# Kernel tuning notes

Hardware: AMD Instinct MI355X
Metric: run time of the kernel (lower is better)

Reference implementation:

```python
import jax, jax.numpy as jnp
import numpy as np
from jax import lax

B, S, D, H = 2, 2048, 1024, 16
DH = D // H
KERNELS = (3, 5)
NK = len(KERNELS)
COUT = D // NK  # channels per conv branch


def setup_inputs() -> dict:
    key = jax.random.key(0)
    ks = jax.random.split(key, 12)
    w = lambda k, shp: (jax.random.normal(k, shp, dtype=jnp.float32) * 0.02)
    inp = {
        "q": jax.random.normal(ks[0], (B, S, D), dtype=jnp.float32),
        "k": jax.random.normal(ks[1], (B, S, D), dtype=jnp.float32),
        "v": jax.random.normal(ks[2], (B, S, D), dtype=jnp.float32),
        "mask": jnp.ones((B, S, S), dtype=jnp.int32),
        "Wq": w(ks[3], (D, D)),
        "Wk": w(ks[4], (D, D)),
        "Wv": w(ks[5], (D, D)),
        "Wo": w(ks[6], (D, D)),
        "bo": jnp.zeros((D,), dtype=jnp.float32),
        "conv_w0": w(ks[7], (COUT, D, KERNELS[0])),  # OIH
        "conv_b0": jnp.zeros((COUT,), dtype=jnp.float32),
        "conv_w1": w(ks[8], (COUT, D, KERNELS[1])),
        "conv_b1": jnp.zeros((COUT,), dtype=jnp.float32),
        "gate": jnp.ones((H,), dtype=jnp.float32),
    }
    return inp


def _split_heads(x):  # [B,S,D] -> [B,H,S,DH]
    return x.reshape(B, S, H, DH).transpose(0, 2, 1, 3)


def _conv1d_same(x_ncl, w_oik, b, ksz):
    pad = ksz // 2
    y = lax.conv_general_dilated(
        x_ncl, w_oik, window_strides=(1,), padding=[(pad, pad)],
        dimension_numbers=("NCH", "OIH", "NCH"))
    return y + b[None, :, None]


def reference(q, k, v, mask, Wq, Wk, Wv, Wo, bo,
              conv_w0, conv_b0, conv_w1, conv_b1, gate):
    qh = _split_heads(q @ Wq.T)
    kh = _split_heads(k @ Wk.T)
    vh = _split_heads(v @ Wv.T)

    # conv-derived K: operate on raw k in NCL layout, concat channel-wise
    k_ncl = k.transpose(0, 2, 1)  # [B,D,S]
    c0 = _conv1d_same(k_ncl, conv_w0, conv_b0, KERNELS[0])
    c1 = _conv1d_same(k_ncl, conv_w1, conv_b1, KERNELS[1])
    k_conv = jnp.concatenate([c0, c1], axis=1).transpose(0, 2, 1)  # [B,S,D]
    kch = _split_heads(k_conv)

    g = jax.nn.sigmoid(gate).reshape(1, H, 1, 1)
    scale = 1.0 / np.sqrt(DH).astype(np.float32)
    attn = ((1.0 - g) * jnp.einsum("bhqd,bhkd->bhqk", qh, kh)
            + g * jnp.einsum("bhqd,bhkd->bhqk", qh, kch)) * scale
    attn = jnp.where(mask[:, None, :, :] == 0, jnp.float32(-1e9), attn)
    attn = jax.nn.softmax(attn, axis=-1)

    out = jnp.einsum("bhqk,bhkd->bhqd", attn, vh)  # [B,H,S,DH]
    out = out.transpose(0, 2, 1, 3).reshape(B, S, D)
    return out @ Wo.T + bo
```

## Files before the change

kernel.cpp:

```cpp
#include <hip/hip_runtime.h>
#include <math.h>

#define Bb 2
#define Ss 2048
#define Dd 1024
#define Hh 16
#define SP 2052

typedef unsigned short u16;
typedef __bf16 bf16x8 __attribute__((ext_vector_type(8)));
typedef float f32x4 __attribute__((ext_vector_type(4)));
typedef unsigned short u16x8 __attribute__((ext_vector_type(8)));

__device__ __forceinline__ u16 f2bf(float f) {
    union { float f; unsigned int u; } c; c.f = f;
    unsigned int u = c.u + 0x7FFFu + ((c.u >> 16) & 1u);
    return (u16)(u >> 16);
}

__device__ __forceinline__ u16 f2bfn(float f) {
    __bf16 h = (__bf16)f;
    union { __bf16 h; u16 u; } c; c.h = h;
    return c.u;
}

__device__ __forceinline__ float bf2f(u16 h) {
    union { unsigned int u; float f; } c; c.u = ((unsigned int)h) << 16;
    return c.f;
}

__device__ __forceinline__ void gload16(const void* g, void* l) {
    __builtin_amdgcn_global_load_lds(
        (const __attribute__((address_space(1))) void*)g,
        (__attribute__((address_space(3))) void*)l, 16, 0, 0);
}

#define PREP_WB 28676
#define PREP_IB 6156
#define PREP_MB 1024

__global__ __launch_bounds__(256) void prep_all(
    const float* __restrict__ Wq, const float* __restrict__ Wk,
    const float* __restrict__ Wv, const float* __restrict__ Wo,
    const float* __restrict__ w0, const float* __restrict__ b0,
    const float* __restrict__ w1, const float* __restrict__ b1,
    const float* __restrict__ gate,
    const float* __restrict__ q, const float* __restrict__ k, const float* __restrict__ v,
    const int* __restrict__ mask,
    u16* __restrict__ wqs, u16* __restrict__ wvb, u16* __restrict__ wob,
    u16* __restrict__ Wc0, u16* __restrict__ Wc1, float* __restrict__ bc,
    u16* __restrict__ qbf, u16* __restrict__ kbf, u16* __restrict__ vbf,
    unsigned int* __restrict__ bits, int* __restrict__ rowflags)
{
    int bid = blockIdx.x, tid = threadIdx.x;
    if (bid < PREP_WB) {
        int idx = bid * 256 + tid;
        const int NW = 1024 * 1024;
        if (idx < NW) { wqs[idx] = f2bf(Wq[idx] * 0.18033688011112042f); return; }
        idx -= NW;
        if (idx < NW) { wvb[idx] = f2bf(Wv[idx]); return; }
        idx -= NW;
        if (idx < NW) { wob[idx] = f2bf(Wo[idx]); return; }
        idx -= NW;
        if (idx < 512 * 3072) {
            int c = idx / 3072, rem = idx % 3072, t = rem >> 10, d = rem & 1023;
            float g = 1.f / (1.f + expf(-gate[c >> 6]));
            float vv = g * w0[(c * 1024 + d) * 3 + t];
            if (t == 1) vv += (1.f - g) * Wk[c * 1024 + d];
            Wc0[idx] = f2bf(vv);
            return;
        }
        idx -= 512 * 3072;
        if (idx < 512 * 5120) {
            int c = idx / 5120, rem = idx % 5120, t = rem >> 10, d = rem & 1023;
            int cg = c + 512;
            float g = 1.f / (1.f + expf(-gate[cg >> 6]));
            float vv = g * w1[(c * 1024 + d) * 5 + t];
            if (t == 2) vv += (1.f - g) * Wk[cg * 1024 + d];
            Wc1[idx] = f2bf(vv);
            return;
        }
        idx -= 512 * 5120;
        if (idx < 1024) {
            float g = 1.f / (1.f + expf(-gate[idx >> 6]));
            bc[idx] = g * (idx < 512 ? b0[idx] : b1[idx - 512]);
        }
        return;
    }
    if (bid < PREP_WB + PREP_IB) {
        int idx = (bid - PREP_WB) * 256 + tid;
        const int per = (Bb * SP * Dd) / 8;
        int which = idx / per;
        if (which >= 3) return;
        int e = (idx - which * per) * 8;
        const float* src = which == 0 ? q : which == 1 ? k : v;
        u16* dst = which == 0 ? qbf : which == 1 ? kbf : vbf;
        int rp = e >> 10, col = e & 1023;
        int b = rp / SP, r = rp - b * SP;
        u16x8 o;
        if (r >= 2 && r < SP - 2) {
            const float* s = &src[((size_t)b * Ss + (r - 2)) * Dd + col];
            float4 lo = *(const float4*)s, hi = *(const float4*)(s + 4);
            o[0] = f2bf(lo.x); o[1] = f2bf(lo.y); o[2] = f2bf(lo.z); o[3] = f2bf(lo.w);
            o[4] = f2bf(hi.x); o[5] = f2bf(hi.y); o[6] = f2bf(hi.z); o[7] = f2bf(hi.w);
        } else {
            #pragma unroll
            for (int j = 0; j < 8; j++) o[j] = 0;
        }
        *(u16x8*)&dst[e] = o;
        return;
    }
    {
        int row = (bid - PREP_WB - PREP_IB) * 4 + (tid >> 6);
        int lane = tid & 63;
        const int* mp = mask + (size_t)row * Ss + lane * 32;
        unsigned int w = 0;
        #pragma unroll
        for (int j = 0; j < 32; j += 4) {
            int4 m4 = *(const int4*)&mp[j];
            if (m4.x != 0) w |= 1u << j;
            if (m4.y != 0) w |= 1u << (j + 1);
            if (m4.z != 0) w |= 1u << (j + 2);
            if (m4.w != 0) w |= 1u << (j + 3);
        }
        bits[(size_t)row * 64 + lane] = w;
        int anyz = __any(w != 0xFFFFFFFFu);
        if (lane == 0) rowflags[row] = anyz;
    }
}

__device__ __forceinline__ void run_gemm_job(
    const u16* __restrict__ A, const u16* __restrict__ B, u16* __restrict__ C,
    int strB, int kS, int kL, int mB, int nB, int rO, int Cst,
    u16* As, u16* Bsh, int lane, int wave, int waveM, int waveN)
{
    f32x4 acc[4][4];
    #pragma unroll
    for (int i = 0; i < 4; i++)
        #pragma unroll
        for (int j = 0; j < 4; j++) acc[i][j] = (f32x4){0.f, 0.f, 0.f, 0.f};

    for (int k0 = kS; k0 < kS + kL; k0 += 32) {
        __syncthreads();
        #pragma unroll
        for (int cc = 0; cc < 2; cc++) {
            int rbase = (wave * 2 + cc) * 16;
            int r = rbase + (lane >> 2);
            int gm = mB + r;
            int grow = (gm >> 11) * SP + (gm & 2047) + rO + (k0 >> 10);
            int csrc = (lane & 3) ^ (r & 3) ^ ((r >> 2) & 3);
            gload16(A + (size_t)grow * 1024 + (k0 & 1023) + csrc * 8, &As[rbase * 32]);
            int gn = nB + r;
            gload16(B + (size_t)gn * strB + k0 + csrc * 8, &Bsh[rbase * 32]);
        }
        __syncthreads();

        bf16x8 af[4], bfr[4];
        #pragma unroll
        for (int t = 0; t < 4; t++) {
            int mrow = waveM + t * 16 + (lane & 15);
            int xm = (mrow & 3) ^ ((mrow >> 2) & 3);
            af[t] = *(const bf16x8*)&As[mrow * 32 + (((lane >> 4) ^ xm)) * 8];
            int nrow = waveN + t * 16 + (lane & 15);
            int xn = (nrow & 3) ^ ((nrow >> 2) & 3);
            bfr[t] = *(const bf16x8*)&Bsh[nrow * 32 + (((lane >> 4) ^ xn)) * 8];
        }
        #pragma unroll
        for (int mt = 0; mt < 4; mt++)
            #pragma unroll
            for (int nt = 0; nt < 4; nt++)
                acc[mt][nt] = __builtin_amdgcn_mfma_f32_16x16x32_bf16(
                    af[mt], bfr[nt], acc[mt][nt], 0, 0, 0);
    }

    #pragma unroll
    for (int mt = 0; mt < 4; mt++)
        #pragma unroll
        for (int nt = 0; nt < 4; nt++)
            #pragma unroll
            for (int r = 0; r < 4; r++) {
                int row = mB + waveM + mt * 16 + (lane >> 4) * 4 + r;
                int gcol = nB + waveN + nt * 16 + (lane & 15);
                C[(size_t)row * Cst + gcol] = f2bf(acc[mt][nt][r]);
            }
}

__global__ __launch_bounds__(256) void gemm_multi(
    const u16* __restrict__ qbf, const u16* __restrict__ kbf, const u16* __restrict__ vbf,
    const u16* __restrict__ wqs, const u16* __restrict__ wvb,
    const u16* __restrict__ Wc0, const u16* __restrict__ Wc1,
    u16* __restrict__ Qp, u16* __restrict__ Vp,
    u16* __restrict__ P0a, u16* __restrict__ P0b,
    u16* __restrict__ P1a, u16* __restrict__ P1b, u16* __restrict__ P1c)
{
    __shared__ u16 As[128 * 32];
    __shared__ u16 Bsh[128 * 32];
    int tid = threadIdx.x, lane = tid & 63, wave = tid >> 6;
    int waveM = (wave >> 1) * 64, waveN = (wave & 1) * 64;

    int bid = (blockIdx.x & 7) * 96 + (blockIdx.x >> 3);

    const u16 *A0, *B0; u16 *C0; int sB0, kS0, kL0, mB0, nB0, rO0, Cs0;
    const u16 *A1 = nullptr, *B1 = nullptr; u16 *C1 = nullptr;
    int sB1 = 0, kS1 = 0, kL1 = 0, mB1 = 0, nB1 = 0, rO1 = 0, Cs1 = 0;
    int njobs = 1;

    if (bid < 128) {
        int t = bid;
        A0 = kbf; B0 = Wc0; C0 = P0a; sB0 = 3072; kS0 = 0; kL0 = 2048;
        mB0 = (t >> 2) * 128; nB0 = (t & 3) * 128; rO0 = 1; Cs0 = 512;
    } else if (bid < 256) {
        int t = bid - 128;
        A0 = kbf; B0 = Wc1; C0 = P1a; sB0 = 5120; kS0 = 0; kL0 = 2048;
        mB0 = (t >> 2) * 128; nB0 = (t & 3) * 128; rO0 = 0; Cs0 = 512;
    } else if (bid < 384) {
        int t = bid - 256;
        A0 = kbf; B0 = Wc1; C0 = P1b; sB0 = 5120; kS0 = 2048; kL0 = 2048;
        mB0 = (t >> 2) * 128; nB0 = (t & 3) * 128; rO0 = 0; Cs0 = 512;
    } else if (bid < 512) {
        int t = bid - 384;
        A0 = kbf; B0 = Wc0; C0 = P0b; sB0 = 3072; kS0 = 2048; kL0 = 1024;
        mB0 = (t >> 2) * 128; nB0 = (t & 3) * 128; rO0 = 1; Cs0 = 512;
        A1 = kbf; B1 = Wc1; C1 = P1c; sB1 = 5120; kS1 = 4096; kL1 = 1024;
        mB1 = mB0; nB1 = nB0; rO1 = 0; Cs1 = 512;
        njobs = 2;
    } else {
        int i0 = (bid - 512) * 2, i1 = i0 + 1;
        if (i0 < 256) { A0 = qbf; B0 = wqs; C0 = Qp; }
        else { i0 -= 256; A0 = vbf; B0 = wvb; C0 = Vp; }
        sB0 = 1024; kS0 = 0; kL0 = 1024;
        mB0 = (i0 >> 3) * 128; nB0 = (i0 & 7) * 128; rO0 = 2; Cs0 = 1024;
        if (i1 < 256) { A1 = qbf; B1 = wqs; C1 = Qp; }
        else { i1 -= 256; A1 = vbf; B1 = wvb; C1 = Vp; }
        sB1 = 1024; kS1 = 0; kL1 = 1024;
        mB1 = (i1 >> 3) * 128; nB1 = (i1 & 7) * 128; rO1 = 2; Cs1 = 1024;
        njobs = 2;
    }

    run_gemm_job(A0, B0, C0, sB0, kS0, kL0, mB0, nB0, rO0, Cs0,
                 As, Bsh, lane, wave, waveM, waveN);
    if (njobs == 2)
        run_gemm_job(A1, B1, C1, sB1, kS1, kL1, mB1, nB1, rO1, Cs1,
                     As, Bsh, lane, wave, waveM, waveN);
}

__global__ __launch_bounds__(256) void reduce_trans(
    const u16* __restrict__ P0a, const u16* __restrict__ P0b,
    const u16* __restrict__ P1a, const u16* __restrict__ P1b, const u16* __restrict__ P1c,
    const float* __restrict__ bc, u16* __restrict__ Keff,
    const u16* __restrict__ Vp, u16* __restrict__ Vt)
{
    __shared__ u16 t[64 * 64];
    int bid = blockIdx.x, tid = threadIdx.x;
    if (bid < 1024) {
        int idx = bid * 256 + tid;
        int e = idx * 8;
        int r = e >> 9, c = e & 511;
        u16x8 a0 = *(const u16x8*)&P0a[e];
        u16x8 b0 = *(const u16x8*)&P0b[e];
        u16x8 a1 = *(const u16x8*)&P1a[e];
        u16x8 b1 = *(const u16x8*)&P1b[e];
        u16x8 c1 = *(const u16x8*)&P1c[e];
        float bias0[8], bias1[8];
        *(float4*)&bias0[0] = *(const float4*)&bc[c];
        *(float4*)&bias0[4] = *(const float4*)&bc[c + 4];
        *(float4*)&bias1[0] = *(const float4*)&bc[512 + c];
        *(float4*)&bias1[4] = *(const float4*)&bc[512 + c + 4];
        u16x8 o0, o1;
        #pragma unroll
        for (int j = 0; j < 8; j++) {
            o0[j] = f2bf(bf2f(a0[j]) + bf2f(b0[j]) + bias0[j]);
            o1[j] = f2bf(bf2f(a1[j]) + bf2f(b1[j]) + bf2f(c1[j]) + bias1[j]);
        }
        *(u16x8*)&Keff[(size_t)r * 1024 + c] = o0;
        *(u16x8*)&Keff[(size_t)r * 1024 + 512 + c] = o1;
        return;
    }
    {
        int vb = bid - 1024;
        int st = vb & 31, h = (vb >> 5) & 15, b = vb >> 9;
        int s0 = st * 64;
        #pragma unroll
        for (int w = 0; w < 2; w++) {
            int f = tid + w * 256;
            int row = f >> 3, c = f & 7;
            int p = c ^ (row & 7);
            u16x8 vv = *(const u16x8*)&Vp[(size_t)(b * Ss + s0 + row) * Dd + h * 64 + c * 8];
            *(u16x8*)&t[row * 64 + p * 8] = vv;
        }
        __syncthreads();
        size_t tbase = (size_t)((b * Hh + h) * 32 + st) * 4096;
        #pragma unroll
        for (int w = 0; w < 2; w++) {
            int f = tid + w * 256;
            int d = f >> 3, c = f & 7;
            int s8 = c * 8;
            u16x8 vv;
            #pragma unroll
            for (int j = 0; j < 8; j++) {
                int s = s8 + j;
                vv[j] = t[s * 64 + (((d >> 3) ^ (s & 7))) * 8 + (d & 7)];
            }
            *(u16x8*)&Vt[tbase + (size_t)d * 64 + ((c ^ (d & 7)) * 8)] = vv;
        }
    }
}

__global__ __launch_bounds__(256) void gemm_out(
    const u16* __restrict__ A, const u16* __restrict__ Bw,
    float* __restrict__ Cf32, const float* __restrict__ bias)
{
    __shared__ u16 As[128 * 32];
    __shared__ u16 Bs[128 * 32];
    int tid = threadIdx.x, lane = tid & 63, wave = tid >> 6;
    int waveM = (wave >> 1) * 64, waveN = (wave & 1) * 64;
    int mBase = blockIdx.y * 128, nBase = blockIdx.x * 128;
    const int K = 1024;

    f32x4 acc[4][4];
    #pragma unroll
    for (int i = 0; i < 4; i++)
        #pragma unroll
        for (int j = 0; j < 4; j++) acc[i][j] = (f32x4){0.f, 0.f, 0.f, 0.f};

    for (int k0 = 0; k0 < K; k0 += 32) {
        __syncthreads();
        #pragma unroll
        for (int cc = 0; cc < 2; cc++) {
            int rbase = (wave * 2 + cc) * 16;
            int r = rbase + (lane >> 2);
            int gm = mBase + r;
            int grow = (gm >> 11) * SP + (gm & 2047) + 2;
            int csrc = (lane & 3) ^ (r & 3) ^ ((r >> 2) & 3);
            gload16(A + (size_t)grow * 1024 + k0 + csrc * 8, &As[rbase * 32]);
            int gn = nBase + r;
            gload16(Bw + (size_t)gn * K + k0 + csrc * 8, &Bs[rbase * 32]);
        }
        __syncthreads();

        bf16x8 af[4], bfr[4];
        #pragma unroll
        for (int t = 0; t < 4; t++) {
            int mrow = waveM + t * 16 + (lane & 15);
            int xm = (mrow & 3) ^ ((mrow >> 2) & 3);
            af[t] = *(const bf16x8*)&As[mrow * 32 + (((lane >> 4) ^ xm)) * 8];
            int nrow = waveN + t * 16 + (lane & 15);
            int xn = (nrow & 3) ^ ((nrow >> 2) & 3);
            bfr[t] = *(const bf16x8*)&Bs[nrow * 32 + (((lane >> 4) ^ xn)) * 8];
        }
        #pragma unroll
        for (int mt = 0; mt < 4; mt++)
            #pragma unroll
            for (int nt = 0; nt < 4; nt++)
                acc[mt][nt] = __builtin_amdgcn_mfma_f32_16x16x32_bf16(
                    af[mt], bfr[nt], acc[mt][nt], 0, 0, 0);
    }

    #pragma unroll
    for (int mt = 0; mt < 4; mt++)
        #pragma unroll
        for (int nt = 0; nt < 4; nt++)
            #pragma unroll
            for (int r = 0; r < 4; r++) {
                int row = mBase + waveM + mt * 16 + (lane >> 4) * 4 + r;
                int gcol = nBase + waveN + nt * 16 + (lane & 15);
                Cf32[(size_t)row * 1024 + gcol] = acc[mt][nt][r] + bias[gcol];
            }
}

__global__ __launch_bounds__(256) void flash_kernel(
    const u16* __restrict__ Qp, const u16* __restrict__ Keff, const u16* __restrict__ Vt,
    const unsigned int* __restrict__ maskbits, const int* __restrict__ rowflags,
    u16* __restrict__ AO)
{
    __shared__ u16 Qs[128 * 64];
    __shared__ u16 Ks[64 * 64];
    __shared__ u16 Vs[64 * 64];
    __shared__ u16 Ps[4][32 * 64];
    int tid = threadIdx.x, lane = tid & 63, wave = tid >> 6;

    int bid = blockIdx.x;
    int xcd = bid & 7, slot = bid >> 3;
    int grp = xcd * 4 + (slot >> 4);
    int q0 = (slot & 15) * 128;
    int h = grp & 15, b = grp >> 4;

    #pragma unroll
    for (int cc = 0; cc < 4; cc++) {
        int rbase = (wave * 4 + cc) * 8;
        int r = rbase + (lane >> 3);
        int csrc = (lane & 7) ^ (r & 7);
        gload16(Qp + (size_t)(b * Ss + q0 + r) * Dd + h * 64 + csrc * 8, &Qs[rbase * 64]);
    }

    int anyz = 0;
    #pragma unroll
    for (int mt = 0; mt < 2; mt++)
        #pragma unroll
        for (int r = 0; r < 4; r++)
            anyz |= rowflags[b * Ss + q0 + wave * 32 + mt * 16 + (lane >> 4) * 4 + r];
    bool doMask = __any(anyz);

    float lrow[2][4];
    f32x4 oa[2][4];
    #pragma unroll
    for (int mt = 0; mt < 2; mt++) {
        #pragma unroll
        for (int r = 0; r < 4; r++) lrow[mt][r] = 0.f;
        #pragma unroll
        for (int nt = 0; nt < 4; nt++) oa[mt][nt] = (f32x4){0.f, 0.f, 0.f, 0.f};
    }

    __syncthreads();

    bf16x8 qa[2][2];
    #pragma unroll
    for (int mt = 0; mt < 2; mt++)
        #pragma unroll
        for (int ks = 0; ks < 2; ks++) {
            int mr = wave * 32 + mt * 16 + (lane & 15);
            int c = ks * 4 + (lane >> 4);
            qa[mt][ks] = *(const bf16x8*)&Qs[mr * 64 + (c ^ (mr & 7)) * 8];
        }

    const u16* vtiles = Vt + (size_t)((b * Hh + h) * 32) * 4096;

    for (int k0 = 0; k0 < Ss; k0 += 64) {
        #pragma unroll
        for (int cc = 0; cc < 2; cc++) {
            int rbase = (wave * 2 + cc) * 8;
            int r = rbase + (lane >> 3);
            int csrc = (lane & 7) ^ (r & 7);
            gload16(Keff + (size_t)(b * Ss + k0 + r) * Dd + h * 64 + csrc * 8, &Ks[rbase * 64]);
        }
        {
            const u16* vtile = vtiles + (size_t)(k0 >> 6) * 4096;
            #pragma unroll
            for (int cc = 0; cc < 2; cc++) {
                int off = (wave * 2 + cc) * 512;
                gload16(vtile + off + lane * 8, &Vs[off]);
            }
        }
        __syncthreads();

        f32x4 sa[2][4];
        #pragma unroll
        for (int mt = 0; mt < 2; mt++)
            #pragma unroll
            for (int nt = 0; nt < 4; nt++) sa[mt][nt] = (f32x4){0.f, 0.f, 0.f, 0.f};
        bf16x8 kb[4][2];
        #pragma unroll
        for (int nt = 0; nt < 4; nt++)
            #pragma unroll
            for (int ks = 0; ks < 2; ks++) {
                int nr = nt * 16 + (lane & 15);
                int c = ks * 4 + (lane >> 4);
                kb[nt][ks] = *(const bf16x8*)&Ks[nr * 64 + (c ^ (nr & 7)) * 8];
            }
        #pragma unroll
        for (int mt = 0; mt < 2; mt++)
            #pragma unroll
            for (int nt = 0; nt < 4; nt++)
                #pragma unroll
                for (int ks = 0; ks < 2; ks++)
                    sa[mt][nt] = __builtin_amdgcn_mfma_f32_16x16x32_bf16(
                        qa[mt][ks], kb[nt][ks], sa[mt][nt], 0, 0, 0);

        bf16x8 vf[4][2];
        #pragma unroll
        for (int nt = 0; nt < 4; nt++)
            #pragma unroll
            for (int ks = 0; ks < 2; ks++) {
                int d = nt * 16 + (lane & 15);
                int c = ks * 4 + (lane >> 4);
                vf[nt][ks] = *(const bf16x8*)&Vs[d * 64 + ((c ^ (d & 7)) * 8)];
            }

        if (doMask) {
            #pragma unroll
            for (int mt = 0; mt < 2; mt++)
                #pragma unroll
                for (int r = 0; r < 4; r++) {
                    int qrow = q0 + wave * 32 + mt * 16 + (lane >> 4) * 4 + r;
                    const unsigned int* mb = &maskbits[((size_t)b * Ss + qrow) * 64 + (k0 >> 5)];
                    unsigned int w0m = mb[0], w1m = mb[1];
                    #pragma unroll
                    for (int nt = 0; nt < 4; nt++) {
                        int col = nt * 16 + (lane & 15);
                        unsigned int w = (col & 32) ? w1m : w0m;
                        if (!((w >> (col & 31)) & 1u)) sa[mt][nt][r] = -1.442695e9f;
                    }
                }
        }

        #pragma unroll
        for (int mt = 0; mt < 2; mt++)
            #pragma unroll
            for (int r = 0; r < 4; r++) {
                float p0 = __builtin_amdgcn_exp2f(sa[mt][0][r]);
                float p1 = __builtin_amdgcn_exp2f(sa[mt][1][r]);
                float p2 = __builtin_amdgcn_exp2f(sa[mt][2][r]);
                float p3 = __builtin_amdgcn_exp2f(sa[mt][3][r]);
                sa[mt][0][r] = p0; sa[mt][1][r] = p1;
                sa[mt][2][r] = p2; sa[mt][3][r] = p3;
                lrow[mt][r] += (p0 + p1) + (p2 + p3);
            }

        u16* pw = Ps[wave];
        #pragma unroll
        for (int mt = 0; mt < 2; mt++)
            #pragma unroll
            for (int nt = 0; nt < 4; nt++)
                #pragma unroll
                for (int r = 0; r < 4; r++) {
                    int row = mt * 16 + (lane >> 4) * 4 + r;
                    int col = nt * 16 + (lane & 15);
                    pw[row * 64 + (((col >> 3) ^ (row & 7))) * 8 + (col & 7)] =
                        f2bfn(sa[mt][nt][r]);
                }

        bf16x8 pa[2][2];
        #pragma unroll
        for (int mt = 0; mt < 2; mt++)
            #pragma unroll
            for (int ks = 0; ks < 2; ks++) {
                int row = mt * 16 + (lane & 15);
                int c = ks * 4 + (lane >> 4);
                pa[mt][ks] = *(const bf16x8*)&pw[row * 64 + (c ^ (row & 7)) * 8];
            }
        #pragma unroll
        for (int mt = 0; mt < 2; mt++)
            #pragma unroll
            for (int nt = 0; nt < 4; nt++)
                #pragma unroll
                for (int ks = 0; ks < 2; ks++)
                    oa[mt][nt] = __builtin_amdgcn_mfma_f32_16x16x32_bf16(
                        pa[mt][ks], vf[nt][ks], oa[mt][nt], 0, 0, 0);

        __syncthreads();
    }

    #pragma unroll
    for (int mt = 0; mt < 2; mt++)
        #pragma unroll
        for (int r = 0; r < 4; r++) {
            float rs = lrow[mt][r];
            #pragma unroll
            for (int d = 1; d < 16; d <<= 1) rs += __shfl_xor(rs, d, 64);
            float inv = 1.f / rs;
            int qrow = q0 + wave * 32 + mt * 16 + (lane >> 4) * 4 + r;
            size_t rowbase = ((size_t)b * SP + 2 + qrow) * Dd + h * 64;
            #pragma unroll
            for (int nt = 0; nt < 4; nt++)
                AO[rowbase + nt * 16 + (lane & 15)] = f2bfn(oa[mt][nt][r] * inv);
        }
}

extern "C" void kernel_launch(void* const* d_in, const int* in_sizes, int n_in,
                              void* d_out, int out_size, void* d_ws, size_t ws_size,
                              hipStream_t stream)
{
    (void)in_sizes; (void)n_in; (void)out_size; (void)ws_size;
    const float* q    = (const float*)d_in[0];
    const float* k    = (const float*)d_in[1];
    const float* v    = (const float*)d_in[2];
    const int*   mask = (const int*)d_in[3];
    const float* Wq   = (const float*)d_in[4];
    const float* Wk   = (const float*)d_in[5];
    const float* Wv   = (const float*)d_in[6];
    const float* Wo   = (const float*)d_in[7];
    const float* bo   = (const float*)d_in[8];
    const float* w0   = (const float*)d_in[9];
    const float* b0   = (const float*)d_in[10];
    const float* w1   = (const float*)d_in[11];
    const float* b1   = (const float*)d_in[12];
    const float* gate = (const float*)d_in[13];
    float* out = (float*)d_out;

    char* p = (char*)d_ws;
    const size_t nPad = (size_t)Bb * SP * Dd;
    const size_t nBSD = (size_t)Bb * Ss * Dd;
    const size_t nHalf = (size_t)4096 * 512;
    u16* qbf  = (u16*)p;            p += nPad * 2;
    u16* kbf  = (u16*)p;            p += nPad * 2;
    u16* vbf  = (u16*)p;            p += nPad * 2;
    u16* Qp   = (u16*)p;            p += nBSD * 2;
    u16* Keff = (u16*)p;            p += nBSD * 2;
    u16* Vp   = (u16*)p;            p += nBSD * 2;
    u16* Vt   = (u16*)p;            p += nBSD * 2;
    u16* wqs  = (u16*)p;            p += (size_t)Dd * Dd * 2;
    u16* wvb  = (u16*)p;            p += (size_t)Dd * Dd * 2;
    u16* wob  = (u16*)p;            p += (size_t)Dd * Dd * 2;
    u16* Wc0  = (u16*)p;            p += (size_t)512 * 3072 * 2;
    u16* Wc1  = (u16*)p;            p += (size_t)512 * 5120 * 2;
    float* bc = (float*)p;          p += 1024 * 4;
    unsigned int* mbits = (unsigned int*)p; p += (size_t)Bb * Ss * 64 * 4;
    int* rflags = (int*)p;          p += (size_t)Bb * Ss * 4;
    u16* P1a = (u16*)p;             p += nHalf * 2;
    u16* P1b = (u16*)p;             p += nHalf * 2;
    u16* P1c = (u16*)p;             p += nHalf * 2;
    u16* P0a = (u16*)p;             p += nHalf * 2;
    u16* P0b = (u16*)p;             p += nHalf * 2;
    u16* AO = vbf;

    hipLaunchKernelGGL(prep_all, dim3(PREP_WB + PREP_IB + PREP_MB), dim3(256), 0, stream,
                       Wq, Wk, Wv, Wo, w0, b0, w1, b1, gate,
                       q, k, v, mask,
                       wqs, wvb, wob, Wc0, Wc1, bc,
                       qbf, kbf, vbf, mbits, rflags);

    hipLaunchKernelGGL(gemm_multi, dim3(768), dim3(256), 0, stream,
                       qbf, kbf, vbf, wqs, wvb, Wc0, Wc1, Qp, Vp,
                       P0a, P0b, P1a, P1b, P1c);

    hipLaunchKernelGGL(reduce_trans, dim3(2048), dim3(256), 0, stream,
                       P0a, P0b, P1a, P1b, P1c, bc, Keff, Vp, Vt);

    hipLaunchKernelGGL(flash_kernel, dim3(512), dim3(256), 0, stream,
                       Qp, Keff, Vt, mbits, rflags, AO);

    hipLaunchKernelGGL(gemm_out, dim3(8, 32), dim3(256), 0, stream,
                       AO, wob, out, bo);
}
```

Baseline: 339.4 us.

## Write V projection directly in transposed tile layout; shrink output GEMM tiles

The V projection GEMM epilogue now writes straight into the swizzled per-head transposed Vt layout the flash kernel reads. This removes the separate Vp buffer and the LDS transpose half of the reduce kernel, which becomes a pure conv reduction. Separately, the output projection GEMM moves to 64x128 tiles, doubling the grid to 512 blocks for better CU occupancy at the cost of less reuse per block. The Vt epilogue stores are 8-byte scattered writes, which may coalesce worse than the old path.

Result: slower. 361.8 us (+6.6%).

```diff
diff --git a/kernel.cpp b/kernel.cpp
--- a/kernel.cpp
+++ b/kernel.cpp
@@ -11,6 +11,7 @@
 typedef __bf16 bf16x8 __attribute__((ext_vector_type(8)));
 typedef float f32x4 __attribute__((ext_vector_type(4)));
 typedef unsigned short u16x8 __attribute__((ext_vector_type(8)));
+typedef unsigned short u16x4 __attribute__((ext_vector_type(4)));
 
 __device__ __forceinline__ u16 f2bf(float f) {
     union { float f; unsigned int u; } c; c.f = f;
@@ -131,7 +132,7 @@
 
 __device__ __forceinline__ void run_gemm_job(
     const u16* __restrict__ A, const u16* __restrict__ B, u16* __restrict__ C,
-    int strB, int kS, int kL, int mB, int nB, int rO, int Cst,
+    int strB, int kS, int kL, int mB, int nB, int rO, int Cst, int vmode,
     u16* As, u16* Bsh, int lane, int wave, int waveM, int waveN)
 {
     f32x4 acc[4][4];
@@ -173,23 +174,42 @@
                     af[mt], bfr[nt], acc[mt][nt], 0, 0, 0);
     }
 
-    #pragma unroll
-    for (int mt = 0; mt < 4; mt++)
-        #pragma unroll
-        for (int nt = 0; nt < 4; nt++)
-            #pragma unroll
-            for (int r = 0; r < 4; r++) {
-                int row = mB + waveM + mt * 16 + (lane >> 4) * 4 + r;
+    if (!vmode) {
+        #pragma unroll
+        for (int mt = 0; mt < 4; mt++)
+            #pragma unroll
+            for (int nt = 0; nt < 4; nt++)
+                #pragma unroll
+                for (int r = 0; r < 4; r++) {
+                    int row = mB + waveM + mt * 16 + (lane >> 4) * 4 + r;
+                    int gcol = nB + waveN + nt * 16 + (lane & 15);
+                    C[(size_t)row * Cst + gcol] = f2bf(acc[mt][nt][r]);
+                }
+    } else {
+        #pragma unroll
+        for (int mt = 0; mt < 4; mt++)
+            #pragma unroll
+            for (int nt = 0; nt < 4; nt++) {
+                int row0 = mB + waveM + mt * 16 + (lane >> 4) * 4;
                 int gcol = nB + waveN + nt * 16 + (lane & 15);
-                C[(size_t)row * Cst + gcol] = f2bf(acc[mt][nt][r]);
+                int b = row0 >> 11, s = row0 & 2047;
+                int st = s >> 6, kv = s & 63;
+                int cch = kv >> 3, j0 = kv & 7;
+                int d = gcol & 63, h = gcol >> 6;
+                u16x4 o;
+                #pragma unroll
+                for (int r = 0; r < 4; r++) o[r] = f2bf(acc[mt][nt][r]);
+                *(u16x4*)&C[((size_t)((b * Hh + h) * 32 + st)) * 4096 +
+                            d * 64 + ((cch ^ (d & 7)) * 8) + j0] = o;
             }
+    }
 }
 
 __global__ __launch_bounds__(256) void gemm_multi(
     const u16* __restrict__ qbf, const u16* __restrict__ kbf, const u16* __restrict__ vbf,
     const u16* __restrict__ wqs, const u16* __restrict__ wvb,
     const u16* __restrict__ Wc0, const u16* __restrict__ Wc1,
-    u16* __restrict__ Qp, u16* __restrict__ Vp,
+    u16* __restrict__ Qp, u16* __restrict__ Vt,
     u16* __restrict__ P0a, u16* __restrict__ P0b,
     u16* __restrict__ P1a, u16* __restrict__ P1b, u16* __restrict__ P1c)
 {
@@ -200,9 +220,9 @@
 
     int bid = (blockIdx.x & 7) * 96 + (blockIdx.x >> 3);
 
-    const u16 *A0, *B0; u16 *C0; int sB0, kS0, kL0, mB0, nB0, rO0, Cs0;
+    const u16 *A0, *B0; u16 *C0; int sB0, kS0, kL0, mB0, nB0, rO0, Cs0, vm0 = 0;
     const u16 *A1 = nullptr, *B1 = nullptr; u16 *C1 = nullptr;
-    int sB1 = 0, kS1 = 0, kL1 = 0, mB1 = 0, nB1 = 0, rO1 = 0, Cs1 = 0;
+    int sB1 = 0, kS1 = 0, kL1 = 0, mB1 = 0, nB1 = 0, rO1 = 0, Cs1 = 0, vm1 = 0;
     int njobs = 1;
 
     if (bid < 128) {
@@ -227,123 +247,96 @@
     } else {
         int i0 = (bid - 512) * 2, i1 = i0 + 1;
         if (i0 < 256) { A0 = qbf; B0 = wqs; C0 = Qp; }
-        else { i0 -= 256; A0 = vbf; B0 = wvb; C0 = Vp; }
+        else { i0 -= 256; A0 = vbf; B0 = wvb; C0 = Vt; vm0 = 1; }
         sB0 = 1024; kS0 = 0; kL0 = 1024;
         mB0 = (i0 >> 3) * 128; nB0 = (i0 & 7) * 128; rO0 = 2; Cs0 = 1024;
         if (i1 < 256) { A1 = qbf; B1 = wqs; C1 = Qp; }
-        else { i1 -= 256; A1 = vbf; B1 = wvb; C1 = Vp; }
+        else { i1 -= 256; A1 = vbf; B1 = wvb; C1 = Vt; vm1 = 1; }
         sB1 = 1024; kS1 = 0; kL1 = 1024;
         mB1 = (i1 >> 3) * 128; nB1 = (i1 & 7) * 128; rO1 = 2; Cs1 = 1024;
         njobs = 2;
     }
 
-    run_gemm_job(A0, B0, C0, sB0, kS0, kL0, mB0, nB0, rO0, Cs0,
+    run_gemm_job(A0, B0, C0, sB0, kS0, kL0, mB0, nB0, rO0, Cs0, vm0,
                  As, Bsh, lane, wave, waveM, waveN);
     if (njobs == 2)
-        run_gemm_job(A1, B1, C1, sB1, kS1, kL1, mB1, nB1, rO1, Cs1,
+        run_gemm_job(A1, B1, C1, sB1, kS1, kL1, mB1, nB1, rO1, Cs1, vm1,
                      As, Bsh, lane, wave, waveM, waveN);
 }
 
-__global__ __launch_bounds__(256) void reduce_trans(
+__global__ __launch_bounds__(256) void conv_reduce(
     const u16* __restrict__ P0a, const u16* __restrict__ P0b,
     const u16* __restrict__ P1a, const u16* __restrict__ P1b, const u16* __restrict__ P1c,
-    const float* __restrict__ bc, u16* __restrict__ Keff,
-    const u16* __restrict__ Vp, u16* __restrict__ Vt)
+    const float* __restrict__ bc, u16* __restrict__ Keff)
 {
-    __shared__ u16 t[64 * 64];
-    int bid = blockIdx.x, tid = threadIdx.x;
-    if (bid < 1024) {
-        int idx = bid * 256 + tid;
-        int e = idx * 8;
-        int r = e >> 9, c = e & 511;
-        u16x8 a0 = *(const u16x8*)&P0a[e];
-        u16x8 b0 = *(const u16x8*)&P0b[e];
-        u16x8 a1 = *(const u16x8*)&P1a[e];
-        u16x8 b1 = *(const u16x8*)&P1b[e];
-        u16x8 c1 = *(const u16x8*)&P1c[e];
-        float bias0[8], bias1[8];
-        *(float4*)&bias0[0] = *(const float4*)&bc[c];
-        *(float4*)&bias0[4] = *(const float4*)&bc[c + 4];
-        *(float4*)&bias1[0] = *(const float4*)&bc[512 + c];
-        *(float4*)&bias1[4] = *(const float4*)&bc[512 + c + 4];
-        u16x8 o0, o1;
-        #pragma unroll
-        for (int j = 0; j < 8; j++) {
-            o0[j] = f2bf(bf2f(a0[j]) + bf2f(b0[j]) + bias0[j]);
-            o1[j] = f2bf(bf2f(a1[j]) + bf2f(b1[j]) + bf2f(c1[j]) + bias1[j]);
-        }
-        *(u16x8*)&Keff[(size_t)r * 1024 + c] = o0;
-        *(u16x8*)&Keff[(size_t)r * 1024 + 512 + c] = o1;
-        return;
-    }
-    {
-        int vb = bid - 1024;
-        int st = vb & 31, h = (vb >> 5) & 15, b = vb >> 9;
-        int s0 = st * 64;
-        #pragma unroll
-        for (int w = 0; w < 2; w++) {
-            int f = tid + w * 256;
-            int row = f >> 3, c = f & 7;
-            int p = c ^ (row & 7);
-            u16x8 vv = *(const u16x8*)&Vp[(size_t)(b * Ss + s0 + row) * Dd + h * 64 + c * 8];
-            *(u16x8*)&t[row * 64 + p * 8] = vv;
-        }
-        __syncthreads();
-        size_t tbase = (size_t)((b * Hh + h) * 32 + st) * 4096;
-        #pragma unroll
-        for (int w = 0; w < 2; w++) {
-            int f = tid + w * 256;
-            int d = f >> 3, c = f & 7;
-            int s8 = c * 8;
-            u16x8 vv;
-            #pragma unroll
-            for (int j = 0; j < 8; j++) {
-                int s = s8 + j;
-                vv[j] = t[s * 64 + (((d >> 3) ^ (s & 7))) * 8 + (d & 7)];
-            }
-            *(u16x8*)&Vt[tbase + (size_t)d * 64 + ((c ^ (d & 7)) * 8)] = vv;
-        }
-    }
+    int idx = blockIdx.x * 256 + threadIdx.x;
+    int e = idx * 8;
+    int r = e >> 9, c = e & 511;
+    u16x8 a0 = *(const u16x8*)&P0a[e];
+    u16x8 b0 = *(const u16x8*)&P0b[e];
+    u16x8 a1 = *(const u16x8*)&P1a[e];
+    u16x8 b1 = *(const u16x8*)&P1b[e];
+    u16x8 c1 = *(const u16x8*)&P1c[e];
+    float bias0[8], bias1[8];
+    *(float4*)&bias0[0] = *(const float4*)&bc[c];
+    *(float4*)&bias0[4] = *(const float4*)&bc[c + 4];
+    *(float4*)&bias1[0] = *(const float4*)&bc[512 + c];
+    *(float4*)&bias1[4] = *(const float4*)&bc[512 + c + 4];
+    u16x8 o0, o1;
+    #pragma unroll
+    for (int j = 0; j < 8; j++) {
+        o0[j] = f2bf(bf2f(a0[j]) + bf2f(b0[j]) + bias0[j]);
+        o1[j] = f2bf(bf2f(a1[j]) + bf2f(b1[j]) + bf2f(c1[j]) + bias1[j]);
+    }
+    *(u16x8*)&Keff[(size_t)r * 1024 + c] = o0;
+    *(u16x8*)&Keff[(size_t)r * 1024 + 512 + c] = o1;
 }
 
 __global__ __launch_bounds__(256) void gemm_out(
     const u16* __restrict__ A, const u16* __restrict__ Bw,
     float* __restrict__ Cf32, const float* __restrict__ bias)
 {
-    __shared__ u16 As[128 * 32];
+    __shared__ u16 As[64 * 32];
     __shared__ u16 Bs[128 * 32];
     int tid = threadIdx.x, lane = tid & 63, wave = tid >> 6;
-    int waveM = (wave >> 1) * 64, waveN = (wave & 1) * 64;
-    int mBase = blockIdx.y * 128, nBase = blockIdx.x * 128;
+    int waveN = wave * 32;
+    int mBase = blockIdx.y * 64, nBase = blockIdx.x * 128;
     const int K = 1024;
 
-    f32x4 acc[4][4];
+    f32x4 acc[4][2];
     #pragma unroll
     for (int i = 0; i < 4; i++)
         #pragma unroll
-        for (int j = 0; j < 4; j++) acc[i][j] = (f32x4){0.f, 0.f, 0.f, 0.f};
+        for (int j = 0; j < 2; j++) acc[i][j] = (f32x4){0.f, 0.f, 0.f, 0.f};
 
     for (int k0 = 0; k0 < K; k0 += 32) {
         __syncthreads();
+        {
+            int r = wave * 16 + (lane >> 2);
+            int gm = mBase + r;
+            int grow = (gm >> 11) * SP + (gm & 2047) + 2;
+            int csrc = (lane & 3) ^ (r & 3) ^ ((r >> 2) & 3);
+            gload16(A + (size_t)grow * 1024 + k0 + csrc * 8, &As[(wave * 16) * 32]);
+        }
         #pragma unroll
         for (int cc = 0; cc < 2; cc++) {
             int rbase = (wave * 2 + cc) * 16;
             int r = rbase + (lane >> 2);
-            int gm = mBase + r;
-            int grow = (gm >> 11) * SP + (gm & 2047) + 2;
+            int gn = nBase + r;
             int csrc = (lane & 3) ^ (r & 3) ^ ((r >> 2) & 3);
-            gload16(A + (size_t)grow * 1024 + k0 + csrc * 8, &As[rbase * 32]);
-            int gn = nBase + r;
             gload16(Bw + (size_t)gn * K + k0 + csrc * 8, &Bs[rbase * 32]);
         }
         __syncthreads();
 
-        bf16x8 af[4], bfr[4];
+        bf16x8 af[4], bfr[2];
         #pragma unroll
         for (int t = 0; t < 4; t++) {
-            int mrow = waveM + t * 16 + (lane & 15);
+            int mrow = t * 16 + (lane & 15);
             int xm = (mrow & 3) ^ ((mrow >> 2) & 3);
             af[t] = *(const bf16x8*)&As[mrow * 32 + (((lane >> 4) ^ xm)) * 8];
+        }
+        #pragma unroll
+        for (int t = 0; t < 2; t++) {
             int nrow = waveN + t * 16 + (lane & 15);
             int xn = (nrow & 3) ^ ((nrow >> 2) & 3);
             bfr[t] = *(const bf16x8*)&Bs[nrow * 32 + (((lane >> 4) ^ xn)) * 8];
@@ -351,7 +344,7 @@
         #pragma unroll
         for (int mt = 0; mt < 4; mt++)
             #pragma unroll
-            for (int nt = 0; nt < 4; nt++)
+            for (int nt = 0; nt < 2; nt++)
                 acc[mt][nt] = __builtin_amdgcn_mfma_f32_16x16x32_bf16(
                     af[mt], bfr[nt], acc[mt][nt], 0, 0, 0);
     }
@@ -359,10 +352,10 @@
     #pragma unroll
     for (int mt = 0; mt < 4; mt++)
         #pragma unroll
-        for (int nt = 0; nt < 4; nt++)
+        for (int nt = 0; nt < 2; nt++)
             #pragma unroll
             for (int r = 0; r < 4; r++) {
-                int row = mBase + waveM + mt * 16 + (lane >> 4) * 4 + r;
+                int row = mBase + mt * 16 + (lane >> 4) * 4 + r;
                 int gcol = nBase + waveN + nt * 16 + (lane & 15);
                 Cf32[(size_t)row * 1024 + gcol] = acc[mt][nt][r] + bias[gcol];
             }
@@ -586,7 +579,6 @@
     u16* vbf  = (u16*)p;            p += nPad * 2;
     u16* Qp   = (u16*)p;            p += nBSD * 2;
     u16* Keff = (u16*)p;            p += nBSD * 2;
-    u16* Vp   = (u16*)p;            p += nBSD * 2;
     u16* Vt   = (u16*)p;            p += nBSD * 2;
     u16* wqs  = (u16*)p;            p += (size_t)Dd * Dd * 2;
     u16* wvb  = (u16*)p;            p += (size_t)Dd * Dd * 2;
@@ -610,15 +602,15 @@
                        qbf, kbf, vbf, mbits, rflags);
 
     hipLaunchKernelGGL(gemm_multi, dim3(768), dim3(256), 0, stream,
-                       qbf, kbf, vbf, wqs, wvb, Wc0, Wc1, Qp, Vp,
+                       qbf, kbf, vbf, wqs, wvb, Wc0, Wc1, Qp, Vt,
                        P0a, P0b, P1a, P1b, P1c);
 
-    hipLaunchKernelGGL(reduce_trans, dim3(2048), dim3(256), 0, stream,
-                       P0a, P0b, P1a, P1b, P1c, bc, Keff, Vp, Vt);
+    hipLaunchKernelGGL(conv_reduce, dim3(1024), dim3(256), 0, stream,
+                       P0a, P0b, P1a, P1b, P1c, bc, Keff);
 
     hipLaunchKernelGGL(flash_kernel, dim3(512), dim3(256), 0, stream,
                        Qp, Keff, Vt, mbits, rflags, AO);
 
-    hipLaunchKernelGGL(gemm_out, dim3(8, 32), dim3(256), 0, stream,
+    hipLaunchKernelGGL(gemm_out, dim3(8, 64), dim3(256), 0, stream,
                        AO, wob, out, bo);
 }
```
